# Kernel optimization log

Measured on AMD Instinct MI355X. Metric: run time of the kernel, lower is better.

## Reference

```python
import jax, jax.numpy as jnp
import numpy as np

B, S, HID = 1, 2048, 4096
NH, NKV, HD = 32, 8, 128
EPS = 1e-6
SCALE = HD ** -0.5


def _rope_cos_sin(seq_len, head_dim, base=1000000.0):
    inv_freq = 1.0 / (base ** (np.arange(0, head_dim, 2, dtype=np.float32) / head_dim))
    t = np.arange(seq_len, dtype=np.float32)
    freqs = np.outer(t, inv_freq)                      # [S, HD/2]
    emb = np.concatenate([freqs, freqs], axis=-1)       # [S, HD]
    return jnp.asarray(np.cos(emb))[None], jnp.asarray(np.sin(emb))[None]  # [1,S,HD]


def setup_inputs() -> dict:
    key = jax.random.key(0)
    ks = jax.random.split(key, 8)
    cos, sin = _rope_cos_sin(S, HD)
    inp = {
        "hidden_states": jax.random.normal(ks[0], (B, S, HID), jnp.float32),
        "cos": jnp.broadcast_to(cos, (B, S, HD)),
        "sin": jnp.broadcast_to(sin, (B, S, HD)),
        "Wq": jax.random.normal(ks[1], (NH * HD, HID), jnp.float32) * 0.02,
        "Wk": jax.random.normal(ks[2], (NKV * HD, HID), jnp.float32) * 0.02,
        "Wv": jax.random.normal(ks[3], (NKV * HD, HID), jnp.float32) * 0.02,
        "Wo": jax.random.normal(ks[4], (HID, NH * HD), jnp.float32) * 0.02,
        "q_norm_w": jnp.ones((HD,), jnp.float32),
        "k_norm_w": jnp.ones((HD,), jnp.float32),
    }
    return inp


def _rmsnorm(x, w, eps=EPS):
    var = jnp.mean(jnp.square(x), axis=-1, keepdims=True)
    return x * jax.lax.rsqrt(var + eps) * w


def _rotate_half(x):
    x1, x2 = jnp.split(x, 2, axis=-1)
    return jnp.concatenate([-x2, x1], axis=-1)


def _apply_rope(x, cos, sin):
    # x: [b,s,n,d]; cos/sin: [b,s,d] -> unsqueeze head dim (dim=2)
    c = cos[:, :, None, :]
    s = sin[:, :, None, :]
    return x * c + _rotate_half(x) * s


def reference(hidden_states, cos, sin, Wq, Wk, Wv, Wo, q_norm_w, k_norm_w):
    b, s, _ = hidden_states.shape
    q = (hidden_states @ Wq.T).reshape(b, s, NH, HD)
    k = (hidden_states @ Wk.T).reshape(b, s, NKV, HD)
    v = (hidden_states @ Wv.T).reshape(b, s, NKV, HD)
    # per-head RMSNorm on q and k
    q = _rmsnorm(q, q_norm_w)
    k = _rmsnorm(k, k_norm_w)
    # RoPE
    q = _apply_rope(q, cos, sin)
    k = _apply_rope(k, cos, sin)
    # GQA: expand kv heads to match query heads (group size = NH // NKV)
    g = NH // NKV
    k = jnp.repeat(k, g, axis=2)  # [b,s,NH,d]
    v = jnp.repeat(v, g, axis=2)
    # causal SDPA, layout bsnd
    scores = jnp.einsum("bqhd,bkhd->bhqk", q, k) * SCALE
    causal = jnp.tril(jnp.ones((s, s), dtype=bool))
    scores = jnp.where(causal[None, None], scores, jnp.finfo(scores.dtype).min)
    probs = jax.nn.softmax(scores, axis=-1)
    attn = jnp.einsum("bhqk,bkhd->bqhd", probs, v).reshape(b, s, NH * HD)
    return attn @ Wo.T
```

## Files before the change

kernel.cpp:

```cpp
#include <hip/hip_runtime.h>
#include <hip/hip_bf16.h>
#include <stdint.h>

#define S_LEN 2048
#define HIDD  4096
#define NH    32
#define NKV   8
#define HD    128
#define NQKV  6144
#define ATT_SCALE 0.08838834764831845f
#define LOG2E 1.4426950408889634f

typedef unsigned short u16;
typedef __attribute__((ext_vector_type(8))) short short8;
typedef __attribute__((ext_vector_type(4))) float f32x4;

__device__ __forceinline__ unsigned f2bfbits(float f){
  union{float f; unsigned u;} v; v.f = f;
  return (v.u + 0x7FFFu + ((v.u>>16)&1u)) >> 16;
}
__device__ __forceinline__ unsigned packbf(float a, float b){
  return f2bfbits(a) | (f2bfbits(b)<<16);
}
__device__ __forceinline__ unsigned cvtpk(float lo, float hi){
  unsigned r;
  asm("v_cvt_pk_bf16_f32 %0, %1, %2" : "=v"(r) : "v"(lo), "v"(hi));
  return r;
}

#define GLOAD16(g, l) __builtin_amdgcn_global_load_lds( \
    (__attribute__((address_space(1))) void*)(g), \
    (__attribute__((address_space(3))) void*)(l), 16, 0, 0)

#define VMWAIT(n) asm volatile("s_waitcnt vmcnt(" #n ")" ::: "memory")
#define SCHED0() __builtin_amdgcn_sched_barrier(0)

__global__ __launch_bounds__(256) void cvt_all(const float* __restrict__ hs,
                                               const float* __restrict__ Wq,
                                               const float* __restrict__ Wk,
                                               const float* __restrict__ Wv,
                                               u16* __restrict__ Xb,
                                               u16* __restrict__ WQKV){
  const float* src; u16* dst; int n8;
  switch (blockIdx.y){
    case 0: src = hs; dst = Xb;                        n8 = S_LEN*HIDD/8;    break;
    case 1: src = Wq; dst = WQKV;                      n8 = NH*HD*HIDD/8;    break;
    case 2: src = Wk; dst = WQKV + (size_t)NH*HD*HIDD; n8 = NKV*HD*HIDD/8;   break;
    default:src = Wv; dst = WQKV + (size_t)(NH+NKV)*HD*HIDD; n8 = NKV*HD*HIDD/8; break;
  }
  int i = blockIdx.x*256 + threadIdx.x;
  if (i >= n8) return;
  const float4* p = (const float4*)src;
  float4 a = p[2*i], b = p[2*i+1];
  union { unsigned u[4]; short8 s; } o;
  o.u[0] = packbf(a.x, a.y); o.u[1] = packbf(a.z, a.w);
  o.u[2] = packbf(b.x, b.y); o.u[3] = packbf(b.z, b.w);
  *(short8*)(dst + (size_t)i*8) = o.s;
}

__global__ __launch_bounds__(256) void cvt_bf16(const float* __restrict__ in,
                                                u16* __restrict__ out, int n8){
  int i = blockIdx.x*256 + threadIdx.x;
  if (i >= n8) return;
  const float4* p = (const float4*)in;
  float4 a = p[2*i], b = p[2*i+1];
  union { unsigned u[4]; short8 s; } o;
  o.u[0] = packbf(a.x, a.y); o.u[1] = packbf(a.z, a.w);
  o.u[2] = packbf(b.x, b.y); o.u[3] = packbf(b.z, b.w);
  *(short8*)(out + (size_t)i*8) = o.s;
}

template<int BM, int BN>
__global__ __launch_bounds__(512) void gemm_4ph(const u16* __restrict__ A,
                                                const u16* __restrict__ B,
                                                float* __restrict__ C,
                                                int N, int K, int nbx){
  constexpr int MREP = BM/32;
  constexpr int NF   = BN/64;
  constexpr int AH   = BM/128;
  constexpr int ASZ  = BM*64;
  __shared__ __align__(16) char lds[4*ASZ + 65536];

  const int tid = threadIdx.x;
  const int w = tid>>6, lane = tid&63, ln = lane&15, g = lane>>4;
  const int wm = w>>2, wn = w&3;
  const int swz5 = ((ln>>3)&1)<<5;

  const int nwg = gridDim.x, flat = blockIdx.x;
  const int wg = (flat&7)*(nwg>>3) + (flat>>3);
  const int by = wg/nbx, bx = wg - by*nbx;
  const int m0 = by*BM, n0 = bx*BN;

  const int rs   = ((tid>>6)<<4) + ((tid&63)>>2);
  const int ksrc = ((tid&3)<<3) ^ (((tid>>5)&1)<<4);
  const u16* srcA[AH];
  #pragma unroll
  for (int h=0;h<AH;h++) srcA[h] = A + (size_t)(m0 + h*128 + rs)*K + ksrc;
  const u16* srcB[2];
  #pragma unroll
  for (int h=0;h<2;h++)  srcB[h] = B + (size_t)(n0 + h*128 + rs)*K + ksrc;

  #define AREG(bf,kh) (lds + ((bf)*2 + (kh))*ASZ)
  #define BREG(bf,kh) (lds + 4*ASZ + ((bf)*2 + (kh))*16384)

  #define STAGEPT(t, kh, bf) { const int off_ = (t)*64 + (kh)*32;                 \
    _Pragma("unroll") for (int h=0;h<AH;h++)                                      \
      GLOAD16(srcA[h]+off_, AREG(bf,kh) + h*8192 + w*1024);                       \
    _Pragma("unroll") for (int h=0;h<2;h++)                                       \
      GLOAD16(srcB[h]+off_, BREG(bf,kh) + h*8192 + w*1024); }

  f32x4 acc[MREP][NF];
  #pragma unroll
  for (int m=0;m<MREP;m++)
    #pragma unroll
    for (int n=0;n<NF;n++) acc[m][n] = (f32x4){0.f,0.f,0.f,0.f};
  short8 a_[MREP], b_[NF];

  #define READA(bf,kh) { _Pragma("unroll") for (int m=0;m<MREP;m++)               \
    a_[m] = *(const short8*)(AREG(bf,kh) + (wm*MREP+m)*1024 + ln*64 + ((g*16)^swz5)); }
  #define READB(bf,kh) { _Pragma("unroll") for (int n=0;n<NF;n++)                 \
    b_[n] = *(const short8*)(BREG(bf,kh) + (wn*NF+n)*1024 + ln*64 + ((g*16)^swz5)); }
  #define MFMACLU() { __builtin_amdgcn_s_setprio(1);                              \
    _Pragma("unroll") for (int m=0;m<MREP;m++)                                    \
      _Pragma("unroll") for (int n=0;n<NF;n++)                                    \
        acc[m][n] = __builtin_amdgcn_mfma_f32_16x16x32_bf16(a_[m], b_[n], acc[m][n], 0,0,0); \
    __builtin_amdgcn_s_setprio(0); }
  #define BARR() __builtin_amdgcn_s_barrier()
  #define VM2LP() do{ if constexpr (AH==2) { VMWAIT(8); } else { VMWAIT(6); } }while(0)
  #define VM1LP() do{ if constexpr (AH==2) { VMWAIT(4); } else { VMWAIT(3); } }while(0)

  STAGEPT(0,0,0); STAGEPT(0,1,0); STAGEPT(1,0,1);
  VMWAIT(0); BARR(); SCHED0();

  const int NIT = K>>7;
  #pragma unroll 1
  for (int it=0; it<NIT; ++it){
    const bool last = (it == NIT-1);
    const int t0 = 2*it;
    READA(0,0); READB(0,0); STAGEPT(t0+1, 1, 1);
    MFMACLU();
    SCHED0(); VM2LP(); BARR(); SCHED0();
    READA(0,1); READB(0,1); if (!last) STAGEPT(t0+2, 0, 0);
    MFMACLU();
    SCHED0(); if (last) { VM1LP(); } else { VM2LP(); } BARR(); SCHED0();
    READA(1,0); READB(1,0); if (!last) STAGEPT(t0+2, 1, 0);
    MFMACLU();
    SCHED0(); if (last) { VMWAIT(0); } else { VM2LP(); } BARR(); SCHED0();
    READA(1,1); READB(1,1); if (!last) STAGEPT(t0+3, 0, 1);
    MFMACLU();
    SCHED0(); if (!last) { VM2LP(); } BARR(); SCHED0();
  }

  #pragma unroll
  for (int mi=0; mi<MREP; mi++)
    #pragma unroll
    for (int n=0; n<NF; n++)
      #pragma unroll
      for (int r=0;r<4;r++){
        int row = m0 + (wm*MREP+mi)*16 + g*4 + r;
        int col = n0 + wn*(NF*16) + n*16 + ln;
        C[(size_t)row*N + col] = acc[mi][n][r];
      }
  #undef AREG
  #undef BREG
  #undef STAGEPT
  #undef READA
  #undef READB
  #undef MFMACLU
  #undef BARR
  #undef VM2LP
  #undef VM1LP
}

__global__ __launch_bounds__(256) void norm_rope(const float* __restrict__ QKV,
                                                 const float* __restrict__ cosb,
                                                 const float* __restrict__ sinb,
                                                 const float* __restrict__ qw,
                                                 const float* __restrict__ kw,
                                                 u16* __restrict__ Qn,
                                                 u16* __restrict__ Kn,
                                                 u16* __restrict__ Vt){
  int w = threadIdx.x>>6, lane = threadIdx.x&63;
  int row = blockIdx.x*4 + w;
  int s = row / 48, slot = row - s*48;
  const float* src = QKV + (size_t)s*NQKV + slot*HD;
  float x0 = src[lane], x1 = src[lane+64];
  if (slot < 40){
    float ss = x0*x0 + x1*x1;
    #pragma unroll
    for (int off=1; off<64; off<<=1) ss += __shfl_xor(ss, off, 64);
    float r = rsqrtf(ss*(1.0f/128.0f) + 1e-6f);
    const float* wgt = (slot < 32) ? qw : kw;
    float y0 = x0*r*wgt[lane], y1 = x1*r*wgt[lane+64];
    float c0 = cosb[(size_t)s*HD+lane], c1 = cosb[(size_t)s*HD+lane+64];
    float s0 = sinb[(size_t)s*HD+lane], s1 = sinb[(size_t)s*HD+lane+64];
    float o0 = y0*c0 - y1*s0;
    float o1 = y1*c1 + y0*s1;
    float sc = (slot < 32) ? ATT_SCALE : 1.0f;
    u16* dst = (slot < 32) ? (Qn + ((size_t)slot*S_LEN + s)*HD)
                           : (Kn + ((size_t)(slot-32)*S_LEN + s)*HD);
    dst[lane]    = (u16)f2bfbits(o0*sc);
    dst[lane+64] = (u16)f2bfbits(o1*sc);
  } else {
    int kvh = slot - 40;
    u16* dst = Vt + (size_t)kvh*HD*S_LEN + s;
    dst[(size_t)lane*S_LEN]      = (u16)f2bfbits(x0);
    dst[(size_t)(lane+64)*S_LEN] = (u16)f2bfbits(x1);
  }
}

__global__ __launch_bounds__(256) void flash_attn(const u16* __restrict__ Qn,
                                                  const u16* __restrict__ Kn,
                                                  const u16* __restrict__ Vt,
                                                  u16* __restrict__ O){
  __shared__ u16 Ks[2][64*128];
  __shared__ u16 Vs[2][128*64];

  const int h = blockIdx.y;
  const int w = threadIdx.x>>6, lane = threadIdx.x&63, ln = lane&15, g = lane>>4;
  const int kvh = h>>2;
  const u16* Qh = Qn + (size_t)h*S_LEN*HD;
  const u16* Kh = Kn + (size_t)kvh*S_LEN*HD;
  const u16* Vh = Vt + (size_t)kvh*HD*S_LEN;

  const int krow_w = w*4 + g;
  const int ksw    = ((krow_w)&7)<<4;
  const int kcol   = ((ln*16) ^ ksw) >> 1;
  const int vrow_w = w*8 + (lane>>3);
  const int vsw    = ((lane>>3)&7)<<4;
  const int vcol   = (((lane&7)*16) ^ vsw) >> 1;

  #define STAGE(bufi, t) { \
    int kv0_ = (t)*64; \
    _Pragma("unroll") \
    for (int p=0;p<4;p++){ \
      const u16* ga = Kh + (size_t)(kv0_ + p*16 + krow_w)*HD + kcol; \
      GLOAD16(ga, (char*)&Ks[bufi][0] + p*4096 + w*1024); \
      const u16* gv = Vh + (size_t)(p*32 + vrow_w)*S_LEN + kv0_ + vcol; \
      GLOAD16(gv, (char*)&Vs[bufi][0] + p*4096 + w*1024); \
    } \
  }

  #pragma unroll 1
  for (int ph=0; ph<2; ph++){
    const int qb = ph ? (31 - blockIdx.x) : blockIdx.x;
    const int q0 = qb*64;
    const int qrow = q0 + w*16 + ln;

    short8 qf[4];
    #pragma unroll
    for (int c=0;c<4;c++)
      qf[c] = *(const short8*)(Qh + (size_t)qrow*HD + c*32 + g*8);

    f32x4 ot[8];
    #pragma unroll
    for (int dt=0;dt<8;dt++) ot[dt] = (f32x4){0.f,0.f,0.f,0.f};
    float m_run = -1e30f, l_run = 0.f;

    const int nt = qb + 1;

    STAGE(0, 0);
    __syncthreads();

    for (int t=0; t<nt; ++t){
      const int cur = t&1;
      if (t+1 < nt) STAGE(cur^1, t+1);
      const int kv0 = t*64;

      f32x4 st[4];
      #pragma unroll
      for (int mt=0; mt<4; mt++){
        f32x4 acc = (f32x4){0.f,0.f,0.f,0.f};
        #pragma unroll
        for (int c=0;c<4;c++){
          short8 kf = *(const short8*)((const char*)&Ks[cur][0]
                        + (mt*16+ln)*256 + ((c*64 + g*16) ^ ((ln&7)<<4)));
          acc = __builtin_amdgcn_mfma_f32_16x16x32_bf16(kf, qf[c], acc, 0,0,0);
        }
        st[mt] = acc;
      }

      float p[4][4];
      float mtile = -1e30f;
      if (t < qb){
        #pragma unroll
        for (int mt=0; mt<4; mt++)
          #pragma unroll
          for (int r=0;r<4;r++){
            p[mt][r] = st[mt][r];
            mtile = fmaxf(mtile, st[mt][r]);
          }
      } else {
        #pragma unroll
        for (int mt=0; mt<4; mt++)
          #pragma unroll
          for (int r=0;r<4;r++){
            int kv = kv0 + mt*16 + 4*g + r;
            float sv = (kv <= qrow) ? st[mt][r] : -1e30f;
            p[mt][r] = sv;
            mtile = fmaxf(mtile, sv);
          }
      }
      mtile = fmaxf(mtile, __shfl_xor(mtile, 16, 64));
      mtile = fmaxf(mtile, __shfl_xor(mtile, 32, 64));

      bool defer = __all(mtile <= m_run + 8.0f);
      float m_new = defer ? m_run : fmaxf(m_run, mtile);

      float l_tile = 0.f;
      #pragma unroll
      for (int mt=0; mt<4; mt++)
        #pragma unroll
        for (int r=0;r<4;r++){
          float e = exp2f((p[mt][r] - m_new)*LOG2E);
          p[mt][r] = e;
          l_tile += e;
        }
      l_tile += __shfl_xor(l_tile, 16, 64);
      l_tile += __shfl_xor(l_tile, 32, 64);
      if (defer){
        l_run += l_tile;
      } else {
        float alpha = exp2f((m_run - m_new)*LOG2E);
        l_run = l_run*alpha + l_tile;
        m_run = m_new;
        #pragma unroll
        for (int dt=0;dt<8;dt++) ot[dt] *= alpha;
      }

      short8 pf[2];
      #pragma unroll
      for (int ks2=0; ks2<2; ks2++){
        unsigned pk00 = cvtpk(p[2*ks2  ][0], p[2*ks2  ][1]);
        unsigned pk01 = cvtpk(p[2*ks2  ][2], p[2*ks2  ][3]);
        unsigned pk10 = cvtpk(p[2*ks2+1][0], p[2*ks2+1][1]);
        unsigned pk11 = cvtpk(p[2*ks2+1][2], p[2*ks2+1][3]);
        int src0 = (((2*g  )&3)<<4) | ln;
        int src1 = (((2*g+1)&3)<<4) | ln;
        unsigned t00 = (unsigned)__shfl((int)pk00, src0, 64);
        unsigned t10 = (unsigned)__shfl((int)pk10, src0, 64);
        unsigned t01 = (unsigned)__shfl((int)pk01, src0, 64);
        unsigned t11 = (unsigned)__shfl((int)pk11, src0, 64);
        unsigned u00 = (unsigned)__shfl((int)pk00, src1, 64);
        unsigned u10 = (unsigned)__shfl((int)pk10, src1, 64);
        unsigned u01 = (unsigned)__shfl((int)pk01, src1, 64);
        unsigned u11 = (unsigned)__shfl((int)pk11, src1, 64);
        bool hiv = (g >= 2);
        union { unsigned u[4]; short8 s; } pw;
        pw.u[0] = hiv ? t10 : t00;
        pw.u[1] = hiv ? t11 : t01;
        pw.u[2] = hiv ? u10 : u00;
        pw.u[3] = hiv ? u11 : u01;
        pf[ks2] = pw.s;
      }

      #pragma unroll
      for (int dt=0;dt<8;dt++){
        #pragma unroll
        for (int ks2=0; ks2<2; ks2++){
          short8 vf = *(const short8*)((const char*)&Vs[cur][0]
                        + (dt*16+ln)*128 + ((ks2*64 + g*16) ^ ((ln&7)<<4)));
          ot[dt] = __builtin_amdgcn_mfma_f32_16x16x32_bf16(vf, pf[ks2], ot[dt], 0,0,0);
        }
      }
      __syncthreads();
    }

    float inv = 1.0f / l_run;
    u16* orow = O + (size_t)qrow*(NH*HD) + h*HD;
    #pragma unroll
    for (int dt=0;dt<8;dt++){
      #pragma unroll
      for (int rr=0; rr<4; rr+=2){
        unsigned pkd = cvtpk(ot[dt][rr]*inv, ot[dt][rr+1]*inv);
        *(unsigned*)(orow + dt*16 + g*4 + rr) = pkd;
      }
    }
  }
  #undef STAGE
}

extern "C" void kernel_launch(void* const* d_in, const int* in_sizes, int n_in,
                              void* d_out, int out_size, void* d_ws, size_t ws_size,
                              hipStream_t stream){
  (void)in_sizes; (void)n_in; (void)out_size; (void)ws_size;
  const float* hs   = (const float*)d_in[0];
  const float* cosb = (const float*)d_in[1];
  const float* sinb = (const float*)d_in[2];
  const float* Wq   = (const float*)d_in[3];
  const float* Wk   = (const float*)d_in[4];
  const float* Wv   = (const float*)d_in[5];
  const float* Wo   = (const float*)d_in[6];
  const float* qw   = (const float*)d_in[7];
  const float* kw   = (const float*)d_in[8];
  float* out = (float*)d_out;

  char* ws = (char*)d_ws;
  u16*   Xb    = (u16*)  (ws);
  u16*   WQKV  = (u16*)  (ws + 16777216);
  float* QKV   = (float*)(ws + 67108864);
  u16*   attnB = (u16*)  (ws + 67108864);
  u16*   Qn    = (u16*)  (ws + 117440512);
  u16*   Kn    = (u16*)  (ws + 134217728);
  u16*   Vt    = (u16*)  (ws + 138412032);
  u16*   Wob   = WQKV;

  cvt_all<<<dim3(8192, 4), 256, 0, stream>>>(hs, Wq, Wk, Wv, Xb, WQKV);
  gemm_4ph<256,192><<<256, 512, 0, stream>>>(Xb, WQKV, QKV, NQKV, HIDD, NQKV/192);
  norm_rope<<<(S_LEN*48)/4, 256, 0, stream>>>(QKV, cosb, sinb, qw, kw, Qn, Kn, Vt);
  cvt_bf16<<<(HIDD*NH*HD/8)/256, 256, 0, stream>>>(Wo, Wob, HIDD*NH*HD/8);
  flash_attn<<<dim3(16, NH), 256, 0, stream>>>(Qn, Kn, Vt, attnB);
  gemm_4ph<128,256><<<256, 512, 0, stream>>>(attnB, Wob, out, HIDD, HIDD, HIDD/256);
}
```

Baseline: 332.7 us.

## Store QKV projection in bf16, fold log2e into Q scale, split K/V staging

The QKV GEMM now writes bf16 instead of fp32, halving the intermediate written by the GEMM and read back by norm_rope. The log2(e) factor is folded into the Q scaling so the softmax exponent multiplies are dropped, and the deferred-rescale threshold is adjusted to match. In flash attention, K and V staging are split so the V prefetch is issued after the QK MFMAs, fragment loads are hoisted ahead of the MFMAs, and setprio brackets the MFMA chains. The GEMM also reorders its A/B LDS reads. Rounding QKV to bf16 before the RMSNorm adds a small precision loss.

```diff
diff --git a/kernel.cpp b/kernel.cpp
--- a/kernel.cpp
+++ b/kernel.cpp
@@ -18,6 +18,10 @@
 __device__ __forceinline__ unsigned f2bfbits(float f){
   union{float f; unsigned u;} v; v.f = f;
   return (v.u + 0x7FFFu + ((v.u>>16)&1u)) >> 16;
+}
+__device__ __forceinline__ float bf2f(u16 b){
+  union{unsigned u; float f;} v; v.u = ((unsigned)b)<<16;
+  return v.f;
 }
 __device__ __forceinline__ unsigned packbf(float a, float b){
   return f2bfbits(a) | (f2bfbits(b)<<16);
@@ -70,10 +74,10 @@
   *(short8*)(out + (size_t)i*8) = o.s;
 }
 
-template<int BM, int BN>
+template<int BM, int BN, typename OT>
 __global__ __launch_bounds__(512) void gemm_4ph(const u16* __restrict__ A,
                                                 const u16* __restrict__ B,
-                                                float* __restrict__ C,
+                                                OT* __restrict__ C,
                                                 int N, int K, int nbx){
   constexpr int MREP = BM/32;
   constexpr int NF   = BN/64;
@@ -137,16 +141,16 @@
   for (int it=0; it<NIT; ++it){
     const bool last = (it == NIT-1);
     const int t0 = 2*it;
-    READA(0,0); READB(0,0); STAGEPT(t0+1, 1, 1);
+    READB(0,0); READA(0,0); STAGEPT(t0+1, 1, 1);
     MFMACLU();
     SCHED0(); VM2LP(); BARR(); SCHED0();
-    READA(0,1); READB(0,1); if (!last) STAGEPT(t0+2, 0, 0);
+    READB(0,1); READA(0,1); if (!last) STAGEPT(t0+2, 0, 0);
     MFMACLU();
     SCHED0(); if (last) { VM1LP(); } else { VM2LP(); } BARR(); SCHED0();
-    READA(1,0); READB(1,0); if (!last) STAGEPT(t0+2, 1, 0);
+    READB(1,0); READA(1,0); if (!last) STAGEPT(t0+2, 1, 0);
     MFMACLU();
     SCHED0(); if (last) { VMWAIT(0); } else { VM2LP(); } BARR(); SCHED0();
-    READA(1,1); READB(1,1); if (!last) STAGEPT(t0+3, 0, 1);
+    READB(1,1); READA(1,1); if (!last) STAGEPT(t0+3, 0, 1);
     MFMACLU();
     SCHED0(); if (!last) { VM2LP(); } BARR(); SCHED0();
   }
@@ -159,7 +163,10 @@
       for (int r=0;r<4;r++){
         int row = m0 + (wm*MREP+mi)*16 + g*4 + r;
         int col = n0 + wn*(NF*16) + n*16 + ln;
-        C[(size_t)row*N + col] = acc[mi][n][r];
+        if constexpr (__is_same(OT, u16))
+          C[(size_t)row*N + col] = (u16)f2bfbits(acc[mi][n][r]);
+        else
+          C[(size_t)row*N + col] = acc[mi][n][r];
       }
   #undef AREG
   #undef BREG
@@ -172,7 +179,7 @@
   #undef VM1LP
 }
 
-__global__ __launch_bounds__(256) void norm_rope(const float* __restrict__ QKV,
+__global__ __launch_bounds__(256) void norm_rope(const u16* __restrict__ QKVb,
                                                  const float* __restrict__ cosb,
                                                  const float* __restrict__ sinb,
                                                  const float* __restrict__ qw,
@@ -183,8 +190,8 @@
   int w = threadIdx.x>>6, lane = threadIdx.x&63;
   int row = blockIdx.x*4 + w;
   int s = row / 48, slot = row - s*48;
-  const float* src = QKV + (size_t)s*NQKV + slot*HD;
-  float x0 = src[lane], x1 = src[lane+64];
+  const u16* src = QKVb + (size_t)s*NQKV + slot*HD;
+  float x0 = bf2f(src[lane]), x1 = bf2f(src[lane+64]);
   if (slot < 40){
     float ss = x0*x0 + x1*x1;
     #pragma unroll
@@ -196,7 +203,7 @@
     float s0 = sinb[(size_t)s*HD+lane], s1 = sinb[(size_t)s*HD+lane+64];
     float o0 = y0*c0 - y1*s0;
     float o1 = y1*c1 + y0*s1;
-    float sc = (slot < 32) ? ATT_SCALE : 1.0f;
+    float sc = (slot < 32) ? (ATT_SCALE*LOG2E) : 1.0f;
     u16* dst = (slot < 32) ? (Qn + ((size_t)slot*S_LEN + s)*HD)
                            : (Kn + ((size_t)(slot-32)*S_LEN + s)*HD);
     dst[lane]    = (u16)f2bfbits(o0*sc);
@@ -230,12 +237,18 @@
   const int vsw    = ((lane>>3)&7)<<4;
   const int vcol   = (((lane&7)*16) ^ vsw) >> 1;
 
-  #define STAGE(bufi, t) { \
+  #define STAGE_K(bufi, t) { \
     int kv0_ = (t)*64; \
     _Pragma("unroll") \
     for (int p=0;p<4;p++){ \
       const u16* ga = Kh + (size_t)(kv0_ + p*16 + krow_w)*HD + kcol; \
       GLOAD16(ga, (char*)&Ks[bufi][0] + p*4096 + w*1024); \
+    } \
+  }
+  #define STAGE_V(bufi, t) { \
+    int kv0_ = (t)*64; \
+    _Pragma("unroll") \
+    for (int p=0;p<4;p++){ \
       const u16* gv = Vh + (size_t)(p*32 + vrow_w)*S_LEN + kv0_ + vcol; \
       GLOAD16(gv, (char*)&Vs[bufi][0] + p*4096 + w*1024); \
     } \
@@ -259,26 +272,32 @@
 
     const int nt = qb + 1;
 
-    STAGE(0, 0);
+    STAGE_K(0, 0); STAGE_V(0, 0);
     __syncthreads();
 
     for (int t=0; t<nt; ++t){
       const int cur = t&1;
-      if (t+1 < nt) STAGE(cur^1, t+1);
+      if (t+1 < nt) STAGE_K(cur^1, t+1);
       const int kv0 = t*64;
 
       f32x4 st[4];
       #pragma unroll
       for (int mt=0; mt<4; mt++){
+        short8 kf[4];
+        #pragma unroll
+        for (int c=0;c<4;c++)
+          kf[c] = *(const short8*)((const char*)&Ks[cur][0]
+                      + (mt*16+ln)*256 + ((c*64 + g*16) ^ ((ln&7)<<4)));
         f32x4 acc = (f32x4){0.f,0.f,0.f,0.f};
-        #pragma unroll
-        for (int c=0;c<4;c++){
-          short8 kf = *(const short8*)((const char*)&Ks[cur][0]
-                        + (mt*16+ln)*256 + ((c*64 + g*16) ^ ((ln&7)<<4)));
-          acc = __builtin_amdgcn_mfma_f32_16x16x32_bf16(kf, qf[c], acc, 0,0,0);
-        }
+        __builtin_amdgcn_s_setprio(1);
+        #pragma unroll
+        for (int c=0;c<4;c++)
+          acc = __builtin_amdgcn_mfma_f32_16x16x32_bf16(kf[c], qf[c], acc, 0,0,0);
+        __builtin_amdgcn_s_setprio(0);
         st[mt] = acc;
       }
+
+      if (t+1 < nt) STAGE_V(cur^1, t+1);
 
       float p[4][4];
       float mtile = -1e30f;
@@ -304,7 +323,7 @@
       mtile = fmaxf(mtile, __shfl_xor(mtile, 16, 64));
       mtile = fmaxf(mtile, __shfl_xor(mtile, 32, 64));
 
-      bool defer = __all(mtile <= m_run + 8.0f);
+      bool defer = __all(mtile <= m_run + 11.5416f);
       float m_new = defer ? m_run : fmaxf(m_run, mtile);
 
       float l_tile = 0.f;
@@ -312,7 +331,7 @@
       for (int mt=0; mt<4; mt++)
         #pragma unroll
         for (int r=0;r<4;r++){
-          float e = exp2f((p[mt][r] - m_new)*LOG2E);
+          float e = exp2f(p[mt][r] - m_new);
           p[mt][r] = e;
           l_tile += e;
         }
@@ -321,7 +340,7 @@
       if (defer){
         l_run += l_tile;
       } else {
-        float alpha = exp2f((m_run - m_new)*LOG2E);
+        float alpha = exp2f(m_run - m_new);
         l_run = l_run*alpha + l_tile;
         m_run = m_new;
         #pragma unroll
@@ -356,12 +375,16 @@
 
       #pragma unroll
       for (int dt=0;dt<8;dt++){
-        #pragma unroll
-        for (int ks2=0; ks2<2; ks2++){
-          short8 vf = *(const short8*)((const char*)&Vs[cur][0]
-                        + (dt*16+ln)*128 + ((ks2*64 + g*16) ^ ((ln&7)<<4)));
-          ot[dt] = __builtin_amdgcn_mfma_f32_16x16x32_bf16(vf, pf[ks2], ot[dt], 0,0,0);
-        }
+        short8 vf[2];
+        #pragma unroll
+        for (int ks2=0; ks2<2; ks2++)
+          vf[ks2] = *(const short8*)((const char*)&Vs[cur][0]
+                      + (dt*16+ln)*128 + ((ks2*64 + g*16) ^ ((ln&7)<<4)));
+        __builtin_amdgcn_s_setprio(1);
+        #pragma unroll
+        for (int ks2=0; ks2<2; ks2++)
+          ot[dt] = __builtin_amdgcn_mfma_f32_16x16x32_bf16(vf[ks2], pf[ks2], ot[dt], 0,0,0);
+        __builtin_amdgcn_s_setprio(0);
       }
       __syncthreads();
     }
@@ -377,7 +400,8 @@
       }
     }
   }
-  #undef STAGE
+  #undef STAGE_K
+  #undef STAGE_V
 }
 
 extern "C" void kernel_launch(void* const* d_in, const int* in_sizes, int n_in,
@@ -398,17 +422,17 @@
   char* ws = (char*)d_ws;
   u16*   Xb    = (u16*)  (ws);
   u16*   WQKV  = (u16*)  (ws + 16777216);
-  float* QKV   = (float*)(ws + 67108864);
-  u16*   attnB = (u16*)  (ws + 67108864);
+  u16*   QKVb  = (u16*)  (ws + 67108864);
+  u16*   attnB = (u16*)  (ws + 94371840);
   u16*   Qn    = (u16*)  (ws + 117440512);
   u16*   Kn    = (u16*)  (ws + 134217728);
   u16*   Vt    = (u16*)  (ws + 138412032);
   u16*   Wob   = WQKV;
 
   cvt_all<<<dim3(8192, 4), 256, 0, stream>>>(hs, Wq, Wk, Wv, Xb, WQKV);
-  gemm_4ph<256,192><<<256, 512, 0, stream>>>(Xb, WQKV, QKV, NQKV, HIDD, NQKV/192);
-  norm_rope<<<(S_LEN*48)/4, 256, 0, stream>>>(QKV, cosb, sinb, qw, kw, Qn, Kn, Vt);
+  gemm_4ph<256,192,u16><<<256, 512, 0, stream>>>(Xb, WQKV, QKVb, NQKV, HIDD, NQKV/192);
+  norm_rope<<<(S_LEN*48)/4, 256, 0, stream>>>(QKVb, cosb, sinb, qw, kw, Qn, Kn, Vt);
   cvt_bf16<<<(HIDD*NH*HD/8)/256, 256, 0, stream>>>(Wo, Wob, HIDD*NH*HD/8);
   flash_attn<<<dim3(16, NH), 256, 0, stream>>>(Qn, Kn, Vt, attnB);
-  gemm_4ph<128,256><<<256, 512, 0, stream>>>(attnB, Wob, out, HIDD, HIDD, HIDD/256);
-}
+  gemm_4ph<128,256,float><<<256, 512, 0, stream>>>(attnB, Wob, out, HIDD, HIDD, HIDD/256);
+}
```

Measured after the change: 330.0 us. Within noise of the previous version (-0.8%).
